# Kernel optimization log

Measured on AMD Instinct MI355X. Metric: run time of the kernel, lower is better.

## Reference

```python
import jax, jax.numpy as jnp
import numpy as np

K = 3
KK = K * K


def conv3x3(x, w, b):
    # x: [B,C,H,W], w: [O,C,3,3]
    y = jax.lax.conv_general_dilated(x, w, (1, 1), ((1, 1), (1, 1)),
                                     dimension_numbers=('NCHW', 'OIHW', 'NCHW'))
    return y + b[None, :, None, None]


def deform_conv(x, offset, w, b):
    # torchvision.ops.deform_conv2d, 3x3, pad=1, stride=1, no mask.
    B, C, H, W = x.shape
    off = offset.reshape(B, KK, 2, H, W)  # per kernel tap: (dy, dx)
    ky = jnp.repeat(jnp.arange(K, dtype=x.dtype) - 1, K)  # [9]
    kx = jnp.tile(jnp.arange(K, dtype=x.dtype) - 1, K)
    py = jnp.arange(H, dtype=x.dtype)[None, None, :, None] + ky[None, :, None, None] + off[:, :, 0]
    px = jnp.arange(W, dtype=x.dtype)[None, None, None, :] + kx[None, :, None, None] + off[:, :, 1]
    y0 = jnp.floor(py)
    x0 = jnp.floor(px)
    wy = (py - y0)[:, None]  # [B,1,9,H,W]
    wx = (px - x0)[:, None]
    y0i = y0.astype(jnp.int32)
    x0i = x0.astype(jnp.int32)
    xf = x.reshape(B, C, H * W)

    def corner(yi, xi):
        valid = ((yi >= 0) & (yi < H) & (xi >= 0) & (xi < W))
        idx = jnp.clip(yi, 0, H - 1) * W + jnp.clip(xi, 0, W - 1)  # [B,9,H,W]
        g = jax.vmap(lambda xb, ib: xb[:, ib.reshape(-1)])(xf, idx)  # [B,C,9*H*W]
        return g.reshape(B, C, KK, H, W) * valid[:, None].astype(x.dtype)

    val = (corner(y0i, x0i) * (1 - wy) * (1 - wx)
           + corner(y0i, x0i + 1) * (1 - wy) * wx
           + corner(y0i + 1, x0i) * wy * (1 - wx)
           + corner(y0i + 1, x0i + 1) * wy * wx)  # [B,C,9,H,W]
    out = jnp.einsum('bckhw,ock->bohw', val, w.reshape(w.shape[0], C, KK))
    return out + b[None, :, None, None]


def se_gate(x, w1, b1, w2, b2):
    # global avg pool -> 1x1 conv -> relu -> 1x1 conv -> sigmoid -> scale
    m = x.mean((2, 3))  # [B,C]
    h = jax.nn.relu(jnp.einsum('bc,rc->br', m, w1) + b1)
    g = jax.nn.sigmoid(jnp.einsum('br,cr->bc', h, w2) + b2)
    return x * g[:, :, None, None]


def resize_bilinear(x, oh, ow):
    # F.interpolate(mode='bilinear', align_corners=False)
    B, C, H, W = x.shape

    def coords(n_in, n_out):
        src = (jnp.arange(n_out, dtype=x.dtype) + 0.5) * (n_in / n_out) - 0.5
        src = jnp.clip(src, 0.0, n_in - 1)
        i0 = jnp.floor(src).astype(jnp.int32)
        i1 = jnp.minimum(i0 + 1, n_in - 1)
        return i0, i1, (src - i0).astype(x.dtype)

    y0, y1, wy = coords(H, oh)
    x = x[:, :, y0, :] * (1 - wy)[None, None, :, None] + x[:, :, y1, :] * wy[None, None, :, None]
    c0, c1, wc = coords(W, ow)
    x = x[:, :, :, c0] * (1 - wc)[None, None, None, :] + x[:, :, :, c1] * wc[None, None, None, :]
    return x


def setup_inputs() -> dict:
    key = jax.random.key(0)
    ks = jax.random.split(key, 12)
    B, C, H, W = 4, 64, 128, 128
    L, O, R = 4, 64, 4  # levels, out_channels, reduction=64//16
    d = {
        'x': jax.random.normal(ks[0], (B, C, H, W), jnp.float32),
        'off_w': jax.random.normal(ks[1], (L, 2 * KK, C, 3, 3), jnp.float32) * 0.01,
        'off_b': jax.random.normal(ks[2], (L, 2 * KK), jnp.float32) * 0.01,
        'dc_w': jax.random.normal(ks[3], (L, O, C, 3, 3), jnp.float32) * 0.05,
        'dc_b': jax.random.normal(ks[4], (L, O), jnp.float32) * 0.05,
        'se_w1': jax.random.normal(ks[5], (L, R, O), jnp.float32) * 0.1,
        'se_b1': jax.random.normal(ks[6], (L, R), jnp.float32) * 0.1,
        'se_w2': jax.random.normal(ks[7], (L, O, R), jnp.float32) * 0.1,
        'se_b2': jax.random.normal(ks[8], (L, O), jnp.float32) * 0.1,
        'fuse_w': jax.random.normal(ks[9], (O, L * O), jnp.float32) * 0.05,
        'fuse_b': jax.random.normal(ks[10], (O,), jnp.float32) * 0.05,
    }
    return d


def reference(x, off_w, off_b, dc_w, dc_b, se_w1, se_b1, se_w2, se_b2, fuse_w, fuse_b):
    B, _, H, W = x.shape
    L = off_w.shape[0]
    cur = x
    feats = []
    for i in range(L):
        if i > 0:
            cur = resize_bilinear(cur, cur.shape[2] // 2, cur.shape[3] // 2)
        off = conv3x3(cur, off_w[i], off_b[i])
        cur = deform_conv(cur, off, dc_w[i], dc_b[i])
        cur = se_gate(cur, se_w1[i], se_b1[i], se_w2[i], se_b2[i])
        feats.append(resize_bilinear(cur, H, W))
    for i in range(L - 2, -1, -1):
        feats[i] = feats[i] + feats[i + 1]
    fused = jnp.concatenate(feats, axis=1)  # [B, L*O, H, W]
    return jnp.einsum('bchw,oc->bohw', fused, fuse_w) + fuse_b[None, :, None, None]
```

## Files before the change

kernel.cpp:

```cpp
#include <hip/hip_runtime.h>
#include <hip/hip_bf16.h>
#include <math.h>


constexpr int Bn = 4;

typedef __attribute__((ext_vector_type(8))) short short8;
typedef __attribute__((ext_vector_type(4))) float f32x4;
typedef __attribute__((ext_vector_type(4))) unsigned uint4v;
typedef __attribute__((ext_vector_type(4))) unsigned short ushort4v;

static __device__ __forceinline__ short f2b(float f){
  union { float f; unsigned u; } v; v.f = f;
  unsigned r = v.u + 0x7fffu + ((v.u >> 16) & 1u);
  return (short)(r >> 16);
}
static __device__ __forceinline__ unsigned f2b2(float x, float y){
  union { __hip_bfloat162 h; unsigned u; } cv;
  cv.h = __float22bfloat162_rn(make_float2(x, y));
  return cv.u;
}
static __device__ __forceinline__ float blo(unsigned u){ return __uint_as_float(u << 16); }
static __device__ __forceinline__ float bhi(unsigned u){ return __uint_as_float(u & 0xffff0000u); }

constexpr size_t OFF_CUR   = 0;
constexpr size_t OFF_DC    = OFF_CUR  + 4194304;
constexpr size_t OFF_T0    = OFF_DC   + 4194304;
constexpr size_t OFF_T1    = OFF_T0   + 4194304;
constexpr size_t OFF_T2    = OFF_T1   + 1048576;
constexpr size_t OFF_T3    = OFF_T2   + 262144;
constexpr size_t OFF_WSUMT = OFF_T3   + 65536;
constexpr size_t OFF_DCWT  = OFF_WSUMT + 8192;
constexpr size_t OFF_OWT   = OFF_DCWT  + 73728;
constexpr size_t OFF_SUMS  = OFF_OWT   + 36864;

__global__ void prep_k(const float* __restrict__ dc_w, const float* __restrict__ off_w,
                       const float* __restrict__ fuse_w, float* __restrict__ ws){
  int i = blockIdx.x * 256 + threadIdx.x;
  short* dcwT  = (short*)(ws + OFF_DCWT);
  short* owT   = (short*)(ws + OFF_OWT);
  short* wsumT = (short*)(ws + OFF_WSUMT);
  if (i < 147456){
    int oc = i / 576, r = i % 576, k = r >> 6, c = r & 63;
    dcwT[i] = f2b(dc_w[(oc*64 + c)*9 + k]);
  } else if (i < 147456 + 73728){
    int t = i - 147456;
    int lm = t / 576, l = lm >> 5, m = lm & 31, r = t % 576, k = r >> 6, c = r & 63;
    owT[t] = (m < 18) ? f2b(off_w[((l*18 + m)*64 + c)*9 + k]) : (short)0;
  } else if (i < 147456 + 73728 + 16384){
    int t = i - (147456 + 73728);
    int l = t / 4096, r = t % 4096, o = r / 64, c = r % 64;
    float s = 0.f;
    for (int jl = 0; jl <= l; jl++) s += fuse_w[o*256 + jl*64 + c];
    wsumT[t] = f2b(s);
  } else if (i < 147456 + 73728 + 16384 + 65536){
    ws[OFF_SUMS + (i - (147456 + 73728 + 16384))] = 0.f;
  }
}

__global__ __launch_bounds__(256) void cvt_k(const float* __restrict__ x, unsigned* __restrict__ cur){
  __shared__ float t[64][65];
  int tile = blockIdx.x;
  int b = tile >> 8, p0 = (tile & 255) << 6;
  int tx = threadIdx.x & 63, ty = threadIdx.x >> 6;
  #pragma unroll
  for (int c = ty; c < 64; c += 4)
    t[c][tx] = x[(((size_t)(b << 6) + c) << 14) + p0 + tx];
  __syncthreads();
  int u = threadIdx.x & 31, pr = threadIdx.x >> 5;
  #pragma unroll
  for (int i = 0; i < 8; i++){
    int pp = pr + i*8;
    unsigned v = f2b2(t[2*u][pp], t[2*u + 1][pp]);
    cur[((size_t)(b << 14) + p0 + pp)*32 + u] = v;
  }
}

template<int H, int LVL>
__global__ __launch_bounds__(256, 7) void deform_k(
    const unsigned* __restrict__ cur, const float* __restrict__ ws_all,
    const float* __restrict__ off_bias, const float* __restrict__ dc_bias,
    float* __restrict__ dc, float* __restrict__ sums){
  constexpr int W = H, P = H * W;
  constexpr int PITCHB = 584 * 2;
  constexpr int TPR = W/4, TPB = P/16;
  __shared__ __align__(16) short valA[16][584];
  __shared__ __align__(16) float4 tapW[144];
  __shared__ __align__(8)  unsigned short tapIs[144][4];
  short* patch = &valA[0][0];
  float* offsP = (float*)((char*)&valA[0][0] + 8192);
  const short* owt = (const short*)(ws_all + OFF_OWT) + LVL * 32 * 576;
  const short* dcw = (const short*)(ws_all + OFF_DCWT) + (size_t)LVL * 64 * 576;
  const int tid = threadIdx.x;
  const int wave = tid >> 6, lane = tid & 63;
  const int c0 = lane & 15, quad = lane >> 4, q4 = quad * 4;
  const int b = blockIdx.x / TPB;
  const int rr = blockIdx.x % TPB;
  const int hrow = (rr / TPR) * 4, wcol = (rr % TPR) * 4;
  const unsigned* curu = cur + (size_t)b * P * 32;

  {
    #pragma unroll
    for (int i = 0; i < 3; i++){
      if (i < 2 || quad == 0){
        int p36 = wave*9 + i*4 + quad;
        int r6 = p36 / 6, c6 = p36 - r6*6;
        int yy = hrow - 1 + r6, xx = wcol - 1 + c6;
        bool v = ((unsigned)yy < (unsigned)H) & ((unsigned)xx < (unsigned)W);
        int idx = v ? (yy*W + xx) : 0;
        uint2 d = *(const uint2*)(curu + (size_t)idx*32 + c0*2);
        if (!v){ d.x = 0u; d.y = 0u; }
        *(uint2*)(patch + p36*72 + c0*4) = d;
      }
    }
  }
  __syncthreads();

  {
    const int colw = wave & 1, kh = wave >> 1;
    const char* pb = (const char*)patch + ((c0 >> 2) * 6 + (c0 & 3)) * 144 + quad * 16;
    const short* wrow = owt + (colw*16 + c0)*576 + quad*8;
    f32x4 oacc = {0,0,0,0};
    if (kh == 0){
      #pragma unroll
      for (int kb = 0; kb < 9; kb++){
        const int tap = kb >> 1;
        short8 a  = *(const short8*)(pb + ((tap/3)*864 + (tap%3)*144 + (kb&1)*64));
        short8 bf = *(const short8*)&wrow[kb*32];
        oacc = __builtin_amdgcn_mfma_f32_16x16x32_bf16(a, bf, oacc, 0, 0, 0);
      }
    } else {
      #pragma unroll
      for (int kb = 0; kb < 9; kb++){
        const int kk = 9 + kb, tap = kk >> 1;
        short8 a  = *(const short8*)(pb + ((tap/3)*864 + (tap%3)*144 + (kk&1)*64));
        short8 bf = *(const short8*)&wrow[kk*32];
        oacc = __builtin_amdgcn_mfma_f32_16x16x32_bf16(a, bf, oacc, 0, 0, 0);
      }
    }
    int comp = colw*16 + c0;
    if (comp < 18){
      #pragma unroll
      for (int r = 0; r < 4; r++) offsP[kh*288 + (q4 + r)*18 + comp] = oacc[r];
    }
  }
  __syncthreads();

  if (tid < 144){
    int p = tid / 9, k = tid % 9;
    int h = hrow + (p >> 2), w = wcol + (p & 3);
    float oy = offsP[p*18 + 2*k]     + offsP[288 + p*18 + 2*k]     + off_bias[LVL*18 + 2*k];
    float ox = offsP[p*18 + 2*k + 1] + offsP[288 + p*18 + 2*k + 1] + off_bias[LVL*18 + 2*k + 1];
    float py = (float)(h + k/3 - 1) + oy;
    float px = (float)(w + k%3 - 1) + ox;
    float y0f = floorf(py), x0f = floorf(px);
    float fy = py - y0f, fx = px - x0f;
    int y0 = (int)y0f, x0 = (int)x0f, y1 = y0 + 1, x1 = x0 + 1;
    bool vy0 = (y0 >= 0) & (y0 < H), vy1 = (y1 >= 0) & (y1 < H);
    bool vx0 = (x0 >= 0) & (x0 < W), vx1 = (x1 >= 0) & (x1 < W);
    int y0c = min(max(y0, 0), H-1), y1c = min(max(y1, 0), H-1);
    int x0c = min(max(x0, 0), W-1), x1c = min(max(x1, 0), W-1);
    float gy = 1.f - fy, gx = 1.f - fx;
    tapW[tid] = make_float4((vy0 & vx0) ? gy*gx : 0.f,
                            (vy0 & vx1) ? gy*fx : 0.f,
                            (vy1 & vx0) ? fy*gx : 0.f,
                            (vy1 & vx1) ? fy*fx : 0.f);
    ushort4v ti = { (unsigned short)(y0c*W + x0c), (unsigned short)(y0c*W + x1c),
                    (unsigned short)(y1c*W + x0c), (unsigned short)(y1c*W + x1c) };
    *(ushort4v*)tapIs[tid] = ti;
  }
  __syncthreads();

  {
    const char* curc8 = (const char*)curu + c0*8;
    int T = wave*36 + quad;
    int p = T/9, k = T - p*9;
    #pragma unroll
    for (int i = 0; i < 9; i++){
      float4 wv = tapW[T];
      uint2 tw = *(const uint2*)tapIs[T];
      uint2 u0 = *(const uint2*)(curc8 + ((tw.x & 0xffffu) << 7));
      uint2 u1 = *(const uint2*)(curc8 + ((tw.x >> 16) << 7));
      uint2 u2 = *(const uint2*)(curc8 + ((tw.y & 0xffffu) << 7));
      uint2 u3 = *(const uint2*)(curc8 + ((tw.y >> 16) << 7));
      float a0 = wv.x*blo(u0.x) + wv.y*blo(u1.x) + wv.z*blo(u2.x) + wv.w*blo(u3.x);
      float a1 = wv.x*bhi(u0.x) + wv.y*bhi(u1.x) + wv.z*bhi(u2.x) + wv.w*bhi(u3.x);
      float a2 = wv.x*blo(u0.y) + wv.y*blo(u1.y) + wv.z*blo(u2.y) + wv.w*blo(u3.y);
      float a3 = wv.x*bhi(u0.y) + wv.y*bhi(u1.y) + wv.z*bhi(u2.y) + wv.w*bhi(u3.y);
      uint2 pk; pk.x = f2b2(a0, a1); pk.y = f2b2(a2, a3);
      *(uint2*)((char*)&valA[0][0] + p*PITCHB + k*128 + c0*8) = pk;
      T += 4; k += 4; if (k >= 9){ k -= 9; ++p; }
    }
  }
  __syncthreads();

  const int n = wave*16 + c0;
  float bt2 = dc_bias[LVL*64 + n];
  f32x4 d0 = {bt2, bt2, bt2, bt2}, d1 = {0,0,0,0};
  #pragma unroll
  for (int kb = 0; kb < 9; kb++){
    short8 a  = *(const short8*)&valA[c0][kb*32 + quad*8];
    short8 bf = *(const short8*)&dcw[n*576 + kb*32 + quad*8];
    d0 = __builtin_amdgcn_mfma_f32_16x16x32_bf16(a, bf, d0, 0, 0, 0);
  }
  #pragma unroll
  for (int kb = 9; kb < 18; kb++){
    short8 a  = *(const short8*)&valA[c0][kb*32 + quad*8];
    short8 bf = *(const short8*)&dcw[n*576 + kb*32 + quad*8];
    d1 = __builtin_amdgcn_mfma_f32_16x16x32_bf16(a, bf, d1, 0, 0, 0);
  }
  f32x4 acc;
  #pragma unroll
  for (int r = 0; r < 4; r++) acc[r] = d0[r] + d1[r];
  float* dcb = dc + ((size_t)b*P + (size_t)(hrow + quad)*W + wcol)*64;
  #pragma unroll
  for (int r = 0; r < 4; r++) dcb[r*64 + n] = acc[r];
  float s = acc[0] + acc[1] + acc[2] + acc[3];
  s += __shfl_xor(s, 16);
  s += __shfl_xor(s, 32);
  if (quad == 0) atomicAdd(&sums[(LVL*16 + (blockIdx.x & 15))*256 + (b << 6) + n], s);
}

template<int W, int LVL>
__global__ __launch_bounds__(256) void fuse_gd_k(
    const float* __restrict__ dcv, const float* __restrict__ sums,
    const float* __restrict__ se_w1, const float* __restrict__ se_b1,
    const float* __restrict__ se_w2, const float* __restrict__ se_b2,
    const float* __restrict__ ws_all, float* __restrict__ tmp, unsigned* __restrict__ curn){
  constexpr int P = W * W;
  constexpr bool POOL = (LVL < 3);
  constexpr float invP = 1.f / (float)P;
  __shared__ __align__(16) float fS[64][68];
  __shared__ __align__(16) float gsh[64];
  const short* wsl = (const short*)(ws_all + OFF_WSUMT) + LVL * 4096;
  const int tid = threadIdx.x, wave = tid >> 6, lane = tid & 63;
  const int c0 = lane & 15, quad = lane >> 4, q4 = quad * 4;
  int b, rp = 0, cs = 0;
  if (POOL){
    constexpr int tilesPerB = P / 64, tilesPerRow = W / 32;
    b = blockIdx.x / tilesPerB;
    int r = blockIdx.x % tilesPerB;
    rp = r / tilesPerRow; cs = r % tilesPerRow;
  } else {
    b = (blockIdx.x * 64) / P;
  }

  {
    int sg = tid >> 6, c = tid & 63;
    float part = 0.f;
    #pragma unroll
    for (int s = 0; s < 4; s++) part += sums[(LVL*16 + sg*4 + s)*256 + (b << 6) + c];
    fS[sg][c] = part;
    __syncthreads();
    if (tid < 64){
      int r = tid & 3, j = tid >> 2;
      float hp = 0.f;
      #pragma unroll
      for (int q = 0; q < 4; q++){
        int cq = j*4 + q;
        float m = (fS[0][cq] + fS[1][cq] + fS[2][cq] + fS[3][cq]) * invP;
        hp += m * se_w1[(LVL*4 + r)*64 + cq];
      }
      hp += __shfl_xor(hp, 4);  hp += __shfl_xor(hp, 8);
      hp += __shfl_xor(hp, 16); hp += __shfl_xor(hp, 32);
      float hr = fmaxf(hp + se_b1[LVL*4 + r], 0.f);
      float a = se_b2[LVL*64 + tid];
      #pragma unroll
      for (int r2 = 0; r2 < 4; r2++)
        a += __shfl(hr, r2) * se_w2[(LVL*64 + tid)*4 + r2];
      gsh[tid] = 1.f / (1.f + expf(-a));
    }
    __syncthreads();
  }

  float4 g4 = *(const float4*)&gsh[c0*4];
  #pragma unroll
  for (int i = 0; i < 4; i++){
    int lp = wave*16 + (lane >> 4) + i*4;
    size_t gpix = POOL ? ((size_t)b*P + (size_t)(2*rp + (lp >> 5))*W + cs*32 + (lp & 31))
                       : ((size_t)blockIdx.x*64 + lp);
    float4 d = *(const float4*)&dcv[gpix*64 + c0*4];
    float4 v = make_float4(d.x*g4.x, d.y*g4.y, d.z*g4.z, d.w*g4.w);
    *(float4*)&fS[lp][c0*4] = v;
  }
  __syncthreads();
  f32x4 acc[4] = {{0,0,0,0},{0,0,0,0},{0,0,0,0},{0,0,0,0}};
  #pragma unroll
  for (int kb = 0; kb < 2; kb++){
    float4 lo = *(const float4*)&fS[wave*16 + c0][kb*32 + quad*8];
    float4 hi = *(const float4*)&fS[wave*16 + c0][kb*32 + quad*8 + 4];
    uint4v ua = {f2b2(lo.x, lo.y), f2b2(lo.z, lo.w), f2b2(hi.x, hi.y), f2b2(hi.z, hi.w)};
    short8 a = __builtin_bit_cast(short8, ua);
    #pragma unroll
    for (int t = 0; t < 4; t++){
      short8 bf = *(const short8*)&wsl[(t*16 + c0)*64 + kb*32 + quad*8];
      acc[t] = __builtin_amdgcn_mfma_f32_16x16x32_bf16(a, bf, acc[t], 0, 0, 0);
    }
  }
  #pragma unroll
  for (int t = 0; t < 4; t++){
    int n = t*16 + c0;
    size_t plane = ((size_t)(b << 6) + n) * P;
    size_t pix = POOL ? ((size_t)(2*rp + (wave >> 1))*W + cs*32 + (wave & 1)*16 + q4)
                      : ((size_t)(blockIdx.x*64) - (size_t)b*P + wave*16 + q4);
    *(f32x4*)&tmp[plane + pix] = acc[t];
  }
  if constexpr (POOL){
    int j = tid >> 4, uu = tid & 15;
    float4 p0 = *(const float4*)&fS[2*j][uu*4];
    float4 p1 = *(const float4*)&fS[2*j + 1][uu*4];
    float4 p2 = *(const float4*)&fS[32 + 2*j][uu*4];
    float4 p3 = *(const float4*)&fS[33 + 2*j][uu*4];
    float4 av = make_float4(0.25f*(p0.x + p1.x + p2.x + p3.x),
                            0.25f*(p0.y + p1.y + p2.y + p3.y),
                            0.25f*(p0.z + p1.z + p2.z + p3.z),
                            0.25f*(p0.w + p1.w + p2.w + p3.w));
    uint2 pv = make_uint2(f2b2(av.x, av.y), f2b2(av.z, av.w));
    *(uint2*)&curn[((size_t)b*(P/4) + (size_t)rp*(W/2) + cs*16 + j)*32 + uu*2] = pv;
  }
}

__global__ void final_k(const float* __restrict__ ws_all, const float* __restrict__ fuse_bias,
                        float* __restrict__ out){
  int i = blockIdx.x * 256 + threadIdx.x;
  int w = i & 127, h = (i >> 7) & 127, o = (i >> 14) & 63, b = i >> 20;
  float acc = fuse_bias[o] + ws_all[OFF_T0 + (((size_t)(b << 6) + o) << 14) + (h << 7) + w];
  const float* tarr[3] = {ws_all + OFF_T1, ws_all + OFF_T2, ws_all + OFF_T3};
  #pragma unroll
  for (int li = 0; li < 3; li++){
    int l = li + 1, Hl = 128 >> l;
    float scale = 1.0f / (float)(1 << l);
    float sy = fminf(fmaxf((h + 0.5f)*scale - 0.5f, 0.f), (float)(Hl - 1));
    float sx = fminf(fmaxf((w + 0.5f)*scale - 0.5f, 0.f), (float)(Hl - 1));
    int y0 = (int)sy, x0 = (int)sx;
    float fy = sy - y0, fx = sx - x0;
    int y1 = min(y0 + 1, Hl - 1), x1 = min(x0 + 1, Hl - 1);
    const float* tb = tarr[li] + (size_t)((b << 6) + o) * Hl * Hl;
    float v00 = tb[y0*Hl + x0], v01 = tb[y0*Hl + x1];
    float v10 = tb[y1*Hl + x0], v11 = tb[y1*Hl + x1];
    acc += (1.f-fy)*((1.f-fx)*v00 + fx*v01) + fy*((1.f-fx)*v10 + fx*v11);
  }
  out[i] = acc;
}

extern "C" void kernel_launch(void* const* d_in, const int* in_sizes, int n_in,
                              void* d_out, int out_size, void* d_ws, size_t ws_size,
                              hipStream_t stream){
  (void)in_sizes; (void)n_in; (void)out_size; (void)ws_size;
  const float* x      = (const float*)d_in[0];
  const float* off_w  = (const float*)d_in[1];
  const float* off_b  = (const float*)d_in[2];
  const float* dc_w   = (const float*)d_in[3];
  const float* dc_b   = (const float*)d_in[4];
  const float* se_w1  = (const float*)d_in[5];
  const float* se_b1  = (const float*)d_in[6];
  const float* se_w2  = (const float*)d_in[7];
  const float* se_b2  = (const float*)d_in[8];
  const float* fuse_w = (const float*)d_in[9];
  const float* fuse_b = (const float*)d_in[10];
  float* out = (float*)d_out;
  float* ws = (float*)d_ws;
  unsigned* cur = (unsigned*)(ws + OFF_CUR);
  float* dc   = ws + OFF_DC;
  float* tmp[4] = {ws + OFF_T0, ws + OFF_T1, ws + OFF_T2, ws + OFF_T3};
  float* sums = ws + OFF_SUMS;

  prep_k<<<(303104 + 255)/256, 256, 0, stream>>>(dc_w, off_w, fuse_w, ws);
  cvt_k<<<1024, 256, 0, stream>>>(x, cur);

  deform_k<128,0><<<4096, 256, 0, stream>>>(cur, ws, off_b, dc_b, dc, sums);
  fuse_gd_k<128,0><<<1024, 256, 0, stream>>>(dc, sums, se_w1, se_b1, se_w2, se_b2, ws, tmp[0], cur);
  deform_k<64,1><<<1024, 256, 0, stream>>>(cur, ws, off_b, dc_b, dc, sums);
  fuse_gd_k<64,1><<<256, 256, 0, stream>>>(dc, sums, se_w1, se_b1, se_w2, se_b2, ws, tmp[1], cur);
  deform_k<32,2><<<256, 256, 0, stream>>>(cur, ws, off_b, dc_b, dc, sums);
  fuse_gd_k<32,2><<<64, 256, 0, stream>>>(dc, sums, se_w1, se_b1, se_w2, se_b2, ws, tmp[2], cur);
  deform_k<16,3><<<64, 256, 0, stream>>>(cur, ws, off_b, dc_b, dc, sums);
  fuse_gd_k<16,3><<<16, 256, 0, stream>>>(dc, sums, se_w1, se_b1, se_w2, se_b2, ws, tmp[3], nullptr);

  final_k<<<16384, 256, 0, stream>>>(ws, fuse_b, out);
}
```

Before: 238.7 us.

## Prefetch weights into registers and software-pipeline the deform bilinear gathers

Result: no change. 238.6 us (-0.0%).

```diff
diff --git a/kernel.cpp b/kernel.cpp
--- a/kernel.cpp
+++ b/kernel.cpp
@@ -77,7 +77,7 @@
 }
 
 template<int H, int LVL>
-__global__ __launch_bounds__(256, 7) void deform_k(
+__global__ __launch_bounds__(256, 3) void deform_k(
     const unsigned* __restrict__ cur, const float* __restrict__ ws_all,
     const float* __restrict__ off_bias, const float* __restrict__ dc_bias,
     float* __restrict__ dc, float* __restrict__ sums){
@@ -88,7 +88,8 @@
   __shared__ __align__(16) float4 tapW[144];
   __shared__ __align__(8)  unsigned short tapIs[144][4];
   short* patch = &valA[0][0];
-  float* offsP = (float*)((char*)&valA[0][0] + 8192);
+  char*  patchB = (char*)patch;
+  float* offsP = (float*)(patchB + 8192);
   const short* owt = (const short*)(ws_all + OFF_OWT) + LVL * 32 * 576;
   const short* dcw = (const short*)(ws_all + OFF_DCWT) + (size_t)LVL * 64 * 576;
   const int tid = threadIdx.x;
@@ -99,43 +100,64 @@
   const int hrow = (rr / TPR) * 4, wcol = (rr % TPR) * 4;
   const unsigned* curu = cur + (size_t)b * P * 32;
 
+  const int pl = lane >> 3, cq = lane & 7;
+  const int px0 = wave*9 + pl;
+  int yy0 = hrow - 1 + px0/6, xx0 = wcol - 1 + px0%6;
+  bool va0 = ((unsigned)yy0 < (unsigned)H) & ((unsigned)xx0 < (unsigned)W);
+  int idx0 = va0 ? (yy0*W + xx0) : 0;
+  uint4 h0 = *(const uint4*)((const char*)curu + (size_t)idx0*128 + cq*16);
+  const int px1 = wave*9 + 8;
+  int yy1 = hrow - 1 + px1/6, xx1 = wcol - 1 + px1%6;
+  bool va1 = ((unsigned)yy1 < (unsigned)H) & ((unsigned)xx1 < (unsigned)W);
+  int idx1 = va1 ? (yy1*W + xx1) : 0;
+  uint4 h1 = {0,0,0,0};
+  if (pl == 0) h1 = *(const uint4*)((const char*)curu + (size_t)idx1*128 + cq*16);
+
+  short8 wB[9];
   {
+    const short* wrow = owt + ((wave & 1)*16 + c0)*576 + quad*8;
     #pragma unroll
-    for (int i = 0; i < 3; i++){
-      if (i < 2 || quad == 0){
-        int p36 = wave*9 + i*4 + quad;
-        int r6 = p36 / 6, c6 = p36 - r6*6;
-        int yy = hrow - 1 + r6, xx = wcol - 1 + c6;
-        bool v = ((unsigned)yy < (unsigned)H) & ((unsigned)xx < (unsigned)W);
-        int idx = v ? (yy*W + xx) : 0;
-        uint2 d = *(const uint2*)(curu + (size_t)idx*32 + c0*2);
-        if (!v){ d.x = 0u; d.y = 0u; }
-        *(uint2*)(patch + p36*72 + c0*4) = d;
-      }
-    }
+    for (int kb = 0; kb < 9; kb++)
+      wB[kb] = *(const short8*)&wrow[((wave >> 1)*9 + kb)*32];
+  }
+  const int n = wave*16 + c0;
+  short8 wD[18];
+  #pragma unroll
+  for (int kb = 0; kb < 18; kb++)
+    wD[kb] = *(const short8*)&dcw[n*576 + kb*32 + quad*8];
+  const float bt2 = dc_bias[LVL*64 + n];
+  const int tk = tid % 9, tp = tid / 9;
+  float oby = 0.f, obx = 0.f;
+  if (tid < 144){
+    oby = off_bias[LVL*18 + 2*tk];
+    obx = off_bias[LVL*18 + 2*tk + 1];
+  }
+
+  if (!va0){ h0.x = 0; h0.y = 0; h0.z = 0; h0.w = 0; }
+  *(uint4*)(patchB + px0*144 + cq*16) = h0;
+  if (pl == 0){
+    if (!va1){ h1.x = 0; h1.y = 0; h1.z = 0; h1.w = 0; }
+    *(uint4*)(patchB + px1*144 + cq*16) = h1;
   }
   __syncthreads();
 
   {
     const int colw = wave & 1, kh = wave >> 1;
-    const char* pb = (const char*)patch + ((c0 >> 2) * 6 + (c0 & 3)) * 144 + quad * 16;
-    const short* wrow = owt + (colw*16 + c0)*576 + quad*8;
+    const char* pb = patchB + ((c0 >> 2) * 6 + (c0 & 3)) * 144 + quad * 16;
     f32x4 oacc = {0,0,0,0};
     if (kh == 0){
       #pragma unroll
       for (int kb = 0; kb < 9; kb++){
         const int tap = kb >> 1;
-        short8 a  = *(const short8*)(pb + ((tap/3)*864 + (tap%3)*144 + (kb&1)*64));
-        short8 bf = *(const short8*)&wrow[kb*32];
-        oacc = __builtin_amdgcn_mfma_f32_16x16x32_bf16(a, bf, oacc, 0, 0, 0);
+        short8 a = *(const short8*)(pb + ((tap/3)*864 + (tap%3)*144 + (kb&1)*64));
+        oacc = __builtin_amdgcn_mfma_f32_16x16x32_bf16(a, wB[kb], oacc, 0, 0, 0);
       }
     } else {
       #pragma unroll
       for (int kb = 0; kb < 9; kb++){
         const int kk = 9 + kb, tap = kk >> 1;
-        short8 a  = *(const short8*)(pb + ((tap/3)*864 + (tap%3)*144 + (kk&1)*64));
-        short8 bf = *(const short8*)&wrow[kk*32];
-        oacc = __builtin_amdgcn_mfma_f32_16x16x32_bf16(a, bf, oacc, 0, 0, 0);
+        short8 a = *(const short8*)(pb + ((tap/3)*864 + (tap%3)*144 + (kk&1)*64));
+        oacc = __builtin_amdgcn_mfma_f32_16x16x32_bf16(a, wB[kb], oacc, 0, 0, 0);
       }
     }
     int comp = colw*16 + c0;
@@ -147,10 +169,10 @@
   __syncthreads();
 
   if (tid < 144){
-    int p = tid / 9, k = tid % 9;
+    int p = tp, k = tk;
     int h = hrow + (p >> 2), w = wcol + (p & 3);
-    float oy = offsP[p*18 + 2*k]     + offsP[288 + p*18 + 2*k]     + off_bias[LVL*18 + 2*k];
-    float ox = offsP[p*18 + 2*k + 1] + offsP[288 + p*18 + 2*k + 1] + off_bias[LVL*18 + 2*k + 1];
+    float oy = offsP[p*18 + 2*k]     + offsP[288 + p*18 + 2*k]     + oby;
+    float ox = offsP[p*18 + 2*k + 1] + offsP[288 + p*18 + 2*k + 1] + obx;
     float py = (float)(h + k/3 - 1) + oy;
     float px = (float)(w + k%3 - 1) + ox;
     float y0f = floorf(py), x0f = floorf(px);
@@ -173,41 +195,57 @@
 
   {
     const char* curc8 = (const char*)curu + c0*8;
-    int T = wave*36 + quad;
-    int p = T/9, k = T - p*9;
-    #pragma unroll
-    for (int i = 0; i < 9; i++){
-      float4 wv = tapW[T];
-      uint2 tw = *(const uint2*)tapIs[T];
-      uint2 u0 = *(const uint2*)(curc8 + ((tw.x & 0xffffu) << 7));
-      uint2 u1 = *(const uint2*)(curc8 + ((tw.x >> 16) << 7));
-      uint2 u2 = *(const uint2*)(curc8 + ((tw.y & 0xffffu) << 7));
-      uint2 u3 = *(const uint2*)(curc8 + ((tw.y >> 16) << 7));
-      float a0 = wv.x*blo(u0.x) + wv.y*blo(u1.x) + wv.z*blo(u2.x) + wv.w*blo(u3.x);
-      float a1 = wv.x*bhi(u0.x) + wv.y*bhi(u1.x) + wv.z*bhi(u2.x) + wv.w*bhi(u3.x);
-      float a2 = wv.x*blo(u0.y) + wv.y*blo(u1.y) + wv.z*blo(u2.y) + wv.w*blo(u3.y);
-      float a3 = wv.x*bhi(u0.y) + wv.y*bhi(u1.y) + wv.z*bhi(u2.y) + wv.w*bhi(u3.y);
+    const int Tq = wave*36 + quad;
+    int obyte[9];
+    {
+      int p = wave*4, k = quad;
+      #pragma unroll
+      for (int i = 0; i < 9; i++){
+        obyte[i] = p*PITCHB + k*128 + c0*8;
+        k += 4; if (k >= 9){ k -= 9; ++p; }
+      }
+    }
+    uint2 uA[4], uB2[4], uC[4];
+    float4 wv0, wv1, wv2;
+    auto gload = [&](uint2* dst, float4& wvr, int i){
+      uint2 t = *(const uint2*)tapIs[Tq + 4*i];
+      wvr = tapW[Tq + 4*i];
+      dst[0] = *(const uint2*)(curc8 + ((size_t)(t.x & 0xffffu) << 7));
+      dst[1] = *(const uint2*)(curc8 + ((size_t)(t.x >> 16)     << 7));
+      dst[2] = *(const uint2*)(curc8 + ((size_t)(t.y & 0xffffu) << 7));
+      dst[3] = *(const uint2*)(curc8 + ((size_t)(t.y >> 16)     << 7));
+    };
+    auto csamp = [&](const uint2* u, float4 wv, int i){
+      float a0 = wv.x*blo(u[0].x) + wv.y*blo(u[1].x) + wv.z*blo(u[2].x) + wv.w*blo(u[3].x);
+      float a1 = wv.x*bhi(u[0].x) + wv.y*bhi(u[1].x) + wv.z*bhi(u[2].x) + wv.w*bhi(u[3].x);
+      float a2 = wv.x*blo(u[0].y) + wv.y*blo(u[1].y) + wv.z*blo(u[2].y) + wv.w*blo(u[3].y);
+      float a3 = wv.x*bhi(u[0].y) + wv.y*bhi(u[1].y) + wv.z*bhi(u[2].y) + wv.w*bhi(u[3].y);
       uint2 pk; pk.x = f2b2(a0, a1); pk.y = f2b2(a2, a3);
-      *(uint2*)((char*)&valA[0][0] + p*PITCHB + k*128 + c0*8) = pk;
-      T += 4; k += 4; if (k >= 9){ k -= 9; ++p; }
-    }
-  }
-  __syncthreads();
-
-  const int n = wave*16 + c0;
-  float bt2 = dc_bias[LVL*64 + n];
+      *(uint2*)(patchB + obyte[i]) = pk;
+    };
+    gload(uA, wv0, 0); gload(uB2, wv1, 1); gload(uC, wv2, 2);
+    csamp(uA, wv0, 0); gload(uA, wv0, 3);
+    csamp(uB2, wv1, 1); gload(uB2, wv1, 4);
+    csamp(uC, wv2, 2); gload(uC, wv2, 5);
+    csamp(uA, wv0, 3); gload(uA, wv0, 6);
+    csamp(uB2, wv1, 4); gload(uB2, wv1, 7);
+    csamp(uC, wv2, 5); gload(uC, wv2, 8);
+    csamp(uA, wv0, 6);
+    csamp(uB2, wv1, 7);
+    csamp(uC, wv2, 8);
+  }
+  __syncthreads();
+
   f32x4 d0 = {bt2, bt2, bt2, bt2}, d1 = {0,0,0,0};
   #pragma unroll
   for (int kb = 0; kb < 9; kb++){
-    short8 a  = *(const short8*)&valA[c0][kb*32 + quad*8];
-    short8 bf = *(const short8*)&dcw[n*576 + kb*32 + quad*8];
-    d0 = __builtin_amdgcn_mfma_f32_16x16x32_bf16(a, bf, d0, 0, 0, 0);
+    short8 a = *(const short8*)&valA[c0][kb*32 + quad*8];
+    d0 = __builtin_amdgcn_mfma_f32_16x16x32_bf16(a, wD[kb], d0, 0, 0, 0);
   }
   #pragma unroll
   for (int kb = 9; kb < 18; kb++){
-    short8 a  = *(const short8*)&valA[c0][kb*32 + quad*8];
-    short8 bf = *(const short8*)&dcw[n*576 + kb*32 + quad*8];
-    d1 = __builtin_amdgcn_mfma_f32_16x16x32_bf16(a, bf, d1, 0, 0, 0);
+    short8 a = *(const short8*)&valA[c0][kb*32 + quad*8];
+    d1 = __builtin_amdgcn_mfma_f32_16x16x32_bf16(a, wD[kb], d1, 0, 0, 0);
   }
   f32x4 acc;
   #pragma unroll
```

## Process four 4x4 tiles per deform block with register-resident weights and patch-local sampling

Applied to the files above, without the earlier changes.

Measured after the change: 258.9 us. +8.5%, slower.

```diff
diff --git a/kernel.cpp b/kernel.cpp
--- a/kernel.cpp
+++ b/kernel.cpp
@@ -22,6 +22,7 @@
 }
 static __device__ __forceinline__ float blo(unsigned u){ return __uint_as_float(u << 16); }
 static __device__ __forceinline__ float bhi(unsigned u){ return __uint_as_float(u & 0xffff0000u); }
+static __device__ __forceinline__ void pinv(uint4v& x){ asm volatile("" : "+v"(x)); }
 
 constexpr size_t OFF_CUR   = 0;
 constexpr size_t OFF_DC    = OFF_CUR  + 4194304;
@@ -77,148 +78,184 @@
 }
 
 template<int H, int LVL>
-__global__ __launch_bounds__(256, 7) void deform_k(
+__global__ __launch_bounds__(256, 3) void deform_k(
     const unsigned* __restrict__ cur, const float* __restrict__ ws_all,
     const float* __restrict__ off_bias, const float* __restrict__ dc_bias,
     float* __restrict__ dc, float* __restrict__ sums){
   constexpr int W = H, P = H * W;
   constexpr int PITCHB = 584 * 2;
-  constexpr int TPR = W/4, TPB = P/16;
+  constexpr int TPR8 = W/8, TPB8 = P/64;
   __shared__ __align__(16) short valA[16][584];
+  __shared__ __align__(16) char  patchS[64*144];
   __shared__ __align__(16) float4 tapW[144];
   __shared__ __align__(8)  unsigned short tapIs[144][4];
-  short* patch = &valA[0][0];
   float* offsP = (float*)((char*)&valA[0][0] + 8192);
   const short* owt = (const short*)(ws_all + OFF_OWT) + LVL * 32 * 576;
   const short* dcw = (const short*)(ws_all + OFF_DCWT) + (size_t)LVL * 64 * 576;
   const int tid = threadIdx.x;
   const int wave = tid >> 6, lane = tid & 63;
   const int c0 = lane & 15, quad = lane >> 4, q4 = quad * 4;
-  const int b = blockIdx.x / TPB;
-  const int rr = blockIdx.x % TPB;
-  const int hrow = (rr / TPR) * 4, wcol = (rr % TPR) * 4;
+  const int b = blockIdx.x / TPB8;
+  const int rr = blockIdx.x % TPB8;
+  const int hrow8 = (rr / TPR8) * 8, wcol8 = (rr % TPR8) * 8;
   const unsigned* curu = cur + (size_t)b * P * 32;
 
+  uint4v wB[9];
   {
-    #pragma unroll
-    for (int i = 0; i < 3; i++){
-      if (i < 2 || quad == 0){
-        int p36 = wave*9 + i*4 + quad;
-        int r6 = p36 / 6, c6 = p36 - r6*6;
-        int yy = hrow - 1 + r6, xx = wcol - 1 + c6;
-        bool v = ((unsigned)yy < (unsigned)H) & ((unsigned)xx < (unsigned)W);
-        int idx = v ? (yy*W + xx) : 0;
-        uint2 d = *(const uint2*)(curu + (size_t)idx*32 + c0*2);
-        if (!v){ d.x = 0u; d.y = 0u; }
-        *(uint2*)(patch + p36*72 + c0*4) = d;
+    const short* wrow = owt + ((wave & 1)*16 + c0)*576 + quad*8;
+    #pragma unroll
+    for (int kb = 0; kb < 9; kb++)
+      wB[kb] = *(const uint4v*)&wrow[((wave >> 1)*9 + kb)*32];
+    #pragma unroll
+    for (int kb = 0; kb < 9; kb++) pinv(wB[kb]);
+  }
+  const int n = wave*16 + c0;
+  uint4v wD[18];
+  #pragma unroll
+  for (int kb = 0; kb < 18; kb++)
+    wD[kb] = *(const uint4v*)&dcw[n*576 + kb*32 + quad*8];
+  #pragma unroll
+  for (int kb = 0; kb < 18; kb++) pinv(wD[kb]);
+  const float bt2 = dc_bias[LVL*64 + n];
+  const int tk = tid % 9, tp = tid / 9;
+  float oby = 0.f, obx = 0.f;
+  if (tid < 144){
+    oby = off_bias[LVL*18 + 2*tk];
+    obx = off_bias[LVL*18 + 2*tk + 1];
+  }
+  const int pl = lane >> 3, cq = lane & 7;
+
+  #pragma unroll 1
+  for (int t = 0; t < 4; t++){
+    const int srow = hrow8 + (t >> 1)*4, scol = wcol8 + (t & 1)*4;
+    if (t) __syncthreads();
+
+    #pragma unroll
+    for (int i = 0; i < 2; i++){
+      int pp = wave*16 + i*8 + pl;
+      int R = pp >> 3, C = pp & 7;
+      int yy = srow - 2 + R, xx = scol - 2 + C;
+      bool v = ((unsigned)yy < (unsigned)H) & ((unsigned)xx < (unsigned)W);
+      int idx = v ? (yy*W + xx) : 0;
+      uint4 d = *(const uint4*)((const char*)curu + (size_t)idx*128 + cq*16);
+      if (!v){ d.x = 0; d.y = 0; d.z = 0; d.w = 0; }
+      *(uint4*)(patchS + pp*144 + cq*16) = d;
+    }
+    __syncthreads();
+
+    {
+      const int colw = wave & 1, kh = wave >> 1;
+      const char* pb = patchS + (((c0 >> 2) + 1)*8 + (c0 & 3) + 1)*144 + quad*16;
+      f32x4 oacc = {0,0,0,0};
+      if (kh == 0){
+        #pragma unroll
+        for (int kb = 0; kb < 9; kb++){
+          const int tap = kb >> 1;
+          short8 a = *(const short8*)(pb + ((tap/3)*8 + (tap%3))*144 + (kb&1)*64);
+          oacc = __builtin_amdgcn_mfma_f32_16x16x32_bf16(a, __builtin_bit_cast(short8, wB[kb]), oacc, 0, 0, 0);
+        }
+      } else {
+        #pragma unroll
+        for (int kb = 0; kb < 9; kb++){
+          const int kk = 9 + kb, tap = kk >> 1;
+          short8 a = *(const short8*)(pb + ((tap/3)*8 + (tap%3))*144 + (kk&1)*64);
+          oacc = __builtin_amdgcn_mfma_f32_16x16x32_bf16(a, __builtin_bit_cast(short8, wB[kb]), oacc, 0, 0, 0);
+        }
       }
-    }
-  }
-  __syncthreads();
-
-  {
-    const int colw = wave & 1, kh = wave >> 1;
-    const char* pb = (const char*)patch + ((c0 >> 2) * 6 + (c0 & 3)) * 144 + quad * 16;
-    const short* wrow = owt + (colw*16 + c0)*576 + quad*8;
-    f32x4 oacc = {0,0,0,0};
-    if (kh == 0){
+      int comp = colw*16 + c0;
+      if (comp < 18){
+        #pragma unroll
+        for (int r = 0; r < 4; r++) offsP[kh*288 + (q4 + r)*18 + comp] = oacc[r];
+      }
+    }
+    __syncthreads();
+
+    if (tid < 144){
+      int p = tp, k = tk;
+      int h = srow + (p >> 2), w = scol + (p & 3);
+      float oy = offsP[p*18 + 2*k]     + offsP[288 + p*18 + 2*k]     + oby;
+      float ox = offsP[p*18 + 2*k + 1] + offsP[288 + p*18 + 2*k + 1] + obx;
+      float py = (float)(h + k/3 - 1) + oy;
+      float px = (float)(w + k%3 - 1) + ox;
+      float y0f = floorf(py), x0f = floorf(px);
+      float fy = py - y0f, fx = px - x0f;
+      int y0 = (int)y0f, x0 = (int)x0f, y1 = y0 + 1, x1 = x0 + 1;
+      bool vy0 = (y0 >= 0) & (y0 < H), vy1 = (y1 >= 0) & (y1 < H);
+      bool vx0 = (x0 >= 0) & (x0 < W), vx1 = (x1 >= 0) & (x1 < W);
+      int y0c = min(max(y0, 0), H-1), y1c = min(max(y1, 0), H-1);
+      int x0c = min(max(x0, 0), W-1), x1c = min(max(x1, 0), W-1);
+      float gy = 1.f - fy, gx = 1.f - fx;
+      tapW[tid] = make_float4((vy0 & vx0) ? gy*gx : 0.f,
+                              (vy0 & vx1) ? gy*fx : 0.f,
+                              (vy1 & vx0) ? fy*gx : 0.f,
+                              (vy1 & vx1) ? fy*fx : 0.f);
+      int ry = y0 - srow + 2, rx = x0 - scol + 2;
+      if (((unsigned)ry < 7u) & ((unsigned)rx < 7u)){
+        tapIs[tid][0] = (unsigned short)(0x8000u | (ry*8 + rx));
+      } else {
+        tapIs[tid][0] = (unsigned short)(y0c*W + x0c);
+        tapIs[tid][1] = (unsigned short)(y0c*W + x1c);
+        tapIs[tid][2] = (unsigned short)(y1c*W + x0c);
+        tapIs[tid][3] = (unsigned short)(y1c*W + x1c);
+      }
+    }
+    __syncthreads();
+
+    {
+      const char* curc8 = (const char*)curu + c0*8;
+      int T = wave*36 + quad;
+      int p = wave*4, k = quad;
       #pragma unroll
-      for (int kb = 0; kb < 9; kb++){
-        const int tap = kb >> 1;
-        short8 a  = *(const short8*)(pb + ((tap/3)*864 + (tap%3)*144 + (kb&1)*64));
-        short8 bf = *(const short8*)&wrow[kb*32];
-        oacc = __builtin_amdgcn_mfma_f32_16x16x32_bf16(a, bf, oacc, 0, 0, 0);
+      for (int i = 0; i < 9; i++){
+        float4 wv = tapW[T];
+        unsigned short t0 = tapIs[T][0];
+        uint2 u0, u1, u2, u3;
+        if (t0 & 0x8000u){
+          const char* pb2 = patchS + (int)(t0 & 0x7fffu)*144 + c0*8;
+          u0 = *(const uint2*)(pb2);
+          u1 = *(const uint2*)(pb2 + 144);
+          u2 = *(const uint2*)(pb2 + 144*8);
+          u3 = *(const uint2*)(pb2 + 144*9);
+        } else {
+          uint2 tw = *(const uint2*)tapIs[T];
+          u0 = *(const uint2*)(curc8 + ((size_t)(tw.x & 0xffffu) << 7));
+          u1 = *(const uint2*)(curc8 + ((size_t)(tw.x >> 16)     << 7));
+          u2 = *(const uint2*)(curc8 + ((size_t)(tw.y & 0xffffu) << 7));
+          u3 = *(const uint2*)(curc8 + ((size_t)(tw.y >> 16)     << 7));
+        }
+        float a0 = wv.x*blo(u0.x) + wv.y*blo(u1.x) + wv.z*blo(u2.x) + wv.w*blo(u3.x);
+        float a1 = wv.x*bhi(u0.x) + wv.y*bhi(u1.x) + wv.z*bhi(u2.x) + wv.w*bhi(u3.x);
+        float a2 = wv.x*blo(u0.y) + wv.y*blo(u1.y) + wv.z*blo(u2.y) + wv.w*blo(u3.y);
+        float a3 = wv.x*bhi(u0.y) + wv.y*bhi(u1.y) + wv.z*bhi(u2.y) + wv.w*bhi(u3.y);
+        uint2 pk; pk.x = f2b2(a0, a1); pk.y = f2b2(a2, a3);
+        *(uint2*)((char*)&valA[0][0] + p*PITCHB + k*128 + c0*8) = pk;
+        T += 4; k += 4; if (k >= 9){ k -= 9; ++p; }
       }
-    } else {
-      #pragma unroll
-      for (int kb = 0; kb < 9; kb++){
-        const int kk = 9 + kb, tap = kk >> 1;
-        short8 a  = *(const short8*)(pb + ((tap/3)*864 + (tap%3)*144 + (kk&1)*64));
-        short8 bf = *(const short8*)&wrow[kk*32];
-        oacc = __builtin_amdgcn_mfma_f32_16x16x32_bf16(a, bf, oacc, 0, 0, 0);
-      }
-    }
-    int comp = colw*16 + c0;
-    if (comp < 18){
-      #pragma unroll
-      for (int r = 0; r < 4; r++) offsP[kh*288 + (q4 + r)*18 + comp] = oacc[r];
-    }
-  }
-  __syncthreads();
-
-  if (tid < 144){
-    int p = tid / 9, k = tid % 9;
-    int h = hrow + (p >> 2), w = wcol + (p & 3);
-    float oy = offsP[p*18 + 2*k]     + offsP[288 + p*18 + 2*k]     + off_bias[LVL*18 + 2*k];
-    float ox = offsP[p*18 + 2*k + 1] + offsP[288 + p*18 + 2*k + 1] + off_bias[LVL*18 + 2*k + 1];
-    float py = (float)(h + k/3 - 1) + oy;
-    float px = (float)(w + k%3 - 1) + ox;
-    float y0f = floorf(py), x0f = floorf(px);
-    float fy = py - y0f, fx = px - x0f;
-    int y0 = (int)y0f, x0 = (int)x0f, y1 = y0 + 1, x1 = x0 + 1;
-    bool vy0 = (y0 >= 0) & (y0 < H), vy1 = (y1 >= 0) & (y1 < H);
-    bool vx0 = (x0 >= 0) & (x0 < W), vx1 = (x1 >= 0) & (x1 < W);
-    int y0c = min(max(y0, 0), H-1), y1c = min(max(y1, 0), H-1);
-    int x0c = min(max(x0, 0), W-1), x1c = min(max(x1, 0), W-1);
-    float gy = 1.f - fy, gx = 1.f - fx;
-    tapW[tid] = make_float4((vy0 & vx0) ? gy*gx : 0.f,
-                            (vy0 & vx1) ? gy*fx : 0.f,
-                            (vy1 & vx0) ? fy*gx : 0.f,
-                            (vy1 & vx1) ? fy*fx : 0.f);
-    ushort4v ti = { (unsigned short)(y0c*W + x0c), (unsigned short)(y0c*W + x1c),
-                    (unsigned short)(y1c*W + x0c), (unsigned short)(y1c*W + x1c) };
-    *(ushort4v*)tapIs[tid] = ti;
-  }
-  __syncthreads();
-
-  {
-    const char* curc8 = (const char*)curu + c0*8;
-    int T = wave*36 + quad;
-    int p = T/9, k = T - p*9;
-    #pragma unroll
-    for (int i = 0; i < 9; i++){
-      float4 wv = tapW[T];
-      uint2 tw = *(const uint2*)tapIs[T];
-      uint2 u0 = *(const uint2*)(curc8 + ((tw.x & 0xffffu) << 7));
-      uint2 u1 = *(const uint2*)(curc8 + ((tw.x >> 16) << 7));
-      uint2 u2 = *(const uint2*)(curc8 + ((tw.y & 0xffffu) << 7));
-      uint2 u3 = *(const uint2*)(curc8 + ((tw.y >> 16) << 7));
-      float a0 = wv.x*blo(u0.x) + wv.y*blo(u1.x) + wv.z*blo(u2.x) + wv.w*blo(u3.x);
-      float a1 = wv.x*bhi(u0.x) + wv.y*bhi(u1.x) + wv.z*bhi(u2.x) + wv.w*bhi(u3.x);
-      float a2 = wv.x*blo(u0.y) + wv.y*blo(u1.y) + wv.z*blo(u2.y) + wv.w*blo(u3.y);
-      float a3 = wv.x*bhi(u0.y) + wv.y*bhi(u1.y) + wv.z*bhi(u2.y) + wv.w*bhi(u3.y);
-      uint2 pk; pk.x = f2b2(a0, a1); pk.y = f2b2(a2, a3);
-      *(uint2*)((char*)&valA[0][0] + p*PITCHB + k*128 + c0*8) = pk;
-      T += 4; k += 4; if (k >= 9){ k -= 9; ++p; }
-    }
-  }
-  __syncthreads();
-
-  const int n = wave*16 + c0;
-  float bt2 = dc_bias[LVL*64 + n];
-  f32x4 d0 = {bt2, bt2, bt2, bt2}, d1 = {0,0,0,0};
-  #pragma unroll
-  for (int kb = 0; kb < 9; kb++){
-    short8 a  = *(const short8*)&valA[c0][kb*32 + quad*8];
-    short8 bf = *(const short8*)&dcw[n*576 + kb*32 + quad*8];
-    d0 = __builtin_amdgcn_mfma_f32_16x16x32_bf16(a, bf, d0, 0, 0, 0);
-  }
-  #pragma unroll
-  for (int kb = 9; kb < 18; kb++){
-    short8 a  = *(const short8*)&valA[c0][kb*32 + quad*8];
-    short8 bf = *(const short8*)&dcw[n*576 + kb*32 + quad*8];
-    d1 = __builtin_amdgcn_mfma_f32_16x16x32_bf16(a, bf, d1, 0, 0, 0);
-  }
-  f32x4 acc;
-  #pragma unroll
-  for (int r = 0; r < 4; r++) acc[r] = d0[r] + d1[r];
-  float* dcb = dc + ((size_t)b*P + (size_t)(hrow + quad)*W + wcol)*64;
-  #pragma unroll
-  for (int r = 0; r < 4; r++) dcb[r*64 + n] = acc[r];
-  float s = acc[0] + acc[1] + acc[2] + acc[3];
-  s += __shfl_xor(s, 16);
-  s += __shfl_xor(s, 32);
-  if (quad == 0) atomicAdd(&sums[(LVL*16 + (blockIdx.x & 15))*256 + (b << 6) + n], s);
+    }
+    __syncthreads();
+
+    f32x4 d0 = {bt2, bt2, bt2, bt2}, d1 = {0,0,0,0};
+    #pragma unroll
+    for (int kb = 0; kb < 9; kb++){
+      short8 a = *(const short8*)&valA[c0][kb*32 + quad*8];
+      d0 = __builtin_amdgcn_mfma_f32_16x16x32_bf16(a, __builtin_bit_cast(short8, wD[kb]), d0, 0, 0, 0);
+    }
+    #pragma unroll
+    for (int kb = 9; kb < 18; kb++){
+      short8 a = *(const short8*)&valA[c0][kb*32 + quad*8];
+      d1 = __builtin_amdgcn_mfma_f32_16x16x32_bf16(a, __builtin_bit_cast(short8, wD[kb]), d1, 0, 0, 0);
+    }
+    f32x4 acc;
+    #pragma unroll
+    for (int r = 0; r < 4; r++) acc[r] = d0[r] + d1[r];
+    float* dcb = dc + ((size_t)b*P + (size_t)(srow + quad)*W + scol)*64;
+    #pragma unroll
+    for (int r = 0; r < 4; r++) dcb[r*64 + n] = acc[r];
+    float s = acc[0] + acc[1] + acc[2] + acc[3];
+    s += __shfl_xor(s, 16);
+    s += __shfl_xor(s, 32);
+    if (quad == 0) atomicAdd(&sums[(LVL*16 + (blockIdx.x & 15))*256 + (b << 6) + n], s);
+  }
 }
 
 template<int W, int LVL>
@@ -368,13 +405,13 @@
   prep_k<<<(303104 + 255)/256, 256, 0, stream>>>(dc_w, off_w, fuse_w, ws);
   cvt_k<<<1024, 256, 0, stream>>>(x, cur);
 
-  deform_k<128,0><<<4096, 256, 0, stream>>>(cur, ws, off_b, dc_b, dc, sums);
+  deform_k<128,0><<<1024, 256, 0, stream>>>(cur, ws, off_b, dc_b, dc, sums);
   fuse_gd_k<128,0><<<1024, 256, 0, stream>>>(dc, sums, se_w1, se_b1, se_w2, se_b2, ws, tmp[0], cur);
-  deform_k<64,1><<<1024, 256, 0, stream>>>(cur, ws, off_b, dc_b, dc, sums);
+  deform_k<64,1><<<256, 256, 0, stream>>>(cur, ws, off_b, dc_b, dc, sums);
   fuse_gd_k<64,1><<<256, 256, 0, stream>>>(dc, sums, se_w1, se_b1, se_w2, se_b2, ws, tmp[1], cur);
-  deform_k<32,2><<<256, 256, 0, stream>>>(cur, ws, off_b, dc_b, dc, sums);
+  deform_k<32,2><<<64, 256, 0, stream>>>(cur, ws, off_b, dc_b, dc, sums);
   fuse_gd_k<32,2><<<64, 256, 0, stream>>>(dc, sums, se_w1, se_b1, se_w2, se_b2, ws, tmp[2], cur);
-  deform_k<16,3><<<64, 256, 0, stream>>>(cur, ws, off_b, dc_b, dc, sums);
+  deform_k<16,3><<<16, 256, 0, stream>>>(cur, ws, off_b, dc_b, dc, sums);
   fuse_gd_k<16,3><<<16, 256, 0, stream>>>(dc, sums, se_w1, se_b1, se_w2, se_b2, ws, tmp[3], nullptr);
 
   final_k<<<16384, 256, 0, stream>>>(ws, fuse_b, out);
```
